# Performance work log

Hardware: AMD Instinct MI355X
Metric: run time of the kernel (lower is better)

Reference implementation:

```python
import jax, jax.numpy as jnp
import numpy as np

B, H, S, D = 4, 16, 2048, 64

def setup_inputs() -> dict:
    key = jax.random.key(0)
    kq, kk, kv = jax.random.split(key, 3)
    q = jax.random.normal(kq, (B, H, S, D), dtype=jnp.float32)
    k = jax.random.normal(kk, (B, H, S, D), dtype=jnp.float32)
    v = jax.random.normal(kv, (B, H, S, D), dtype=jnp.float32)
    return {"q": q, "k": k, "v": v}

def reference(q, k, v):
    # Faithful port of TransformerBlock.scaled_dot_product_attention
    # (is_causal=True, mha_dropout=0.0 / eval mode).
    head_dim = q.shape[-1]
    scale = jnp.asarray(head_dim, q.dtype) ** -0.5
    q_len, k_len = q.shape[-2], k.shape[-2]
    # causal additive bias: 0 on/below diagonal, -inf above
    causal = jnp.tril(jnp.ones((q_len, k_len), dtype=bool))
    attn_bias = jnp.where(causal, jnp.asarray(0.0, q.dtype), jnp.asarray(-jnp.inf, q.dtype))
    # [b,h,s,d] x [b,h,t,d] -> [b,h,s,t]
    attn_weights = jnp.einsum('bhsd,bhtd->bhst', q * scale, k) + attn_bias
    attn = jax.nn.softmax(attn_weights, axis=-1)
    out = jnp.einsum('bhst,bhtd->bhsd', attn, v)
    return out
```

## Files before the change

kernel.cpp:

```cpp
#include <hip/hip_runtime.h>
#include <math.h>


#define S_LEN 2048
#define D_DIM 64
#define TK 64
#define NHEAD 64
#define MASKV -30000.0f
#define MINIT 1000.0f
#define DEFER_THR 12.0f
#define MNEG -30000.0f
#define LSTR 72
#define PREP_KBLK 1024
#define PREP_VBLK 128

typedef __attribute__((ext_vector_type(8)))  short bf16x8;
typedef __attribute__((ext_vector_type(4)))  float f32x4;
typedef __attribute__((ext_vector_type(16))) float f32x16;

static __device__ __forceinline__ float fast_exp2(float x) {
#if __has_builtin(__builtin_amdgcn_exp2f)
    return __builtin_amdgcn_exp2f(x);
#else
    float r;
    asm volatile("v_exp_f32 %0, %1\n\ts_nop 1" : "=v"(r) : "v"(x));
    return r;
#endif
}

static __device__ __forceinline__ float fmax3(float a, float b, float c) {
    return fmaxf(fmaxf(a, b), c);
}

static __device__ __forceinline__ unsigned int pack_bf16(float a, float b) {
    union { float f; unsigned int u; } ca, cb;
    ca.f = a; cb.f = b;
    unsigned int ua = ca.u + 0x8000u;
    unsigned int ub = cb.u + 0x8000u;
    return (ua >> 16) | (ub & 0xFFFF0000u);
}

static __device__ __forceinline__ unsigned int pack_bf16_fast(float a, float b) {
#if __has_builtin(__builtin_amdgcn_perm)
    union { float f; unsigned int u; } ca, cb;
    ca.f = a; cb.f = b;
    return __builtin_amdgcn_perm(cb.u + 0x8000u, ca.u + 0x8000u, 0x07060302u);
#else
    return pack_bf16(a, b);
#endif
}

static __device__ __forceinline__ void plswap(unsigned int& x, unsigned int& y) {
    asm("s_nop 1\n\tv_permlane32_swap_b32 %0, %1" : "+v"(x), "+v"(y));
}
static __device__ __forceinline__ void plswapf(float x, float& t, float& u) {
    union { float f; unsigned int i; } c;
    c.f = x;
    unsigned int a = c.i, b;
    asm("v_mov_b32 %1, %0\n\t"
        "s_nop 1\n\t"
        "v_permlane32_swap_b32 %0, %1"
        : "+v"(a), "=&v"(b));
    c.i = a; t = c.f;
    c.i = b; u = c.f;
}

typedef const __attribute__((address_space(1))) unsigned int* gas1_t;
typedef __attribute__((address_space(3))) unsigned int* las3_t;
static __device__ __forceinline__ void stage16(const void* g, void* l) {
    __builtin_amdgcn_global_load_lds((gas1_t)g, (las3_t)l, 16, 0, 0);
}

__global__ __launch_bounds__(256)
void fa_prep(const float* __restrict__ kg, const float* __restrict__ vg,
             unsigned short* __restrict__ kb, unsigned short* __restrict__ vb)
{
    const int tid = threadIdx.x;
    const int bid = blockIdx.x;
    if (bid < PREP_KBLK) {
        const int tcid = bid * 256 + tid;
        float4 a[4], b[4];
        int rowv[4], dstv[4];
        #pragma unroll
        for (int s = 0; s < 4; ++s) {
            const int cid = tcid + s * 262144;
            const int ch  = cid & 7;
            const int row = cid >> 3;
            const int kv  = row & (S_LEN - 1);
            const float4* sp = reinterpret_cast<const float4*>(kg + (size_t)row * D_DIM + ch * 8);
            a[s] = sp[0];
            b[s] = sp[1];
            rowv[s] = row;
            dstv[s] = ch ^ (kv & 7);
        }
        #pragma unroll
        for (int s = 0; s < 4; ++s) {
            uint4 w;
            w.x = pack_bf16(a[s].x, a[s].y); w.y = pack_bf16(a[s].z, a[s].w);
            w.z = pack_bf16(b[s].x, b[s].y); w.w = pack_bf16(b[s].z, b[s].w);
            *reinterpret_cast<uint4*>(kb + (size_t)rowv[s] * D_DIM + dstv[s] * 8) = w;
        }
    } else {
        const int wvb  = (bid - PREP_KBLK) * 4 + (tid >> 6);
        const int lane = tid & 63;
        const int kg8  = lane >> 3;
        const int dg   = lane & 7;
        #pragma unroll 1
        for (int s = 0; s < 4; ++s) {
            const int wv = wvb + s * (PREP_VBLK * 4);
            const float* sp = vg + ((size_t)wv * TK + kg8 * 8) * D_DIM + dg * 8;
            float va[8][8];
            #pragma unroll
            for (int i = 0; i < 8; ++i) {
                const float4* q4 = reinterpret_cast<const float4*>(sp + (size_t)i * D_DIM);
                float4 x = q4[0], y = q4[1];
                va[i][0] = x.x; va[i][1] = x.y; va[i][2] = x.z; va[i][3] = x.w;
                va[i][4] = y.x; va[i][5] = y.y; va[i][6] = y.z; va[i][7] = y.w;
            }
            unsigned short* db = vb + (size_t)wv * (TK * D_DIM);
            #pragma unroll
            for (int j = 0; j < 8; ++j) {
                const int d = dg * 8 + j;
                uint4 w;
                w.x = pack_bf16(va[0][j], va[1][j]);
                w.y = pack_bf16(va[2][j], va[3][j]);
                w.z = pack_bf16(va[4][j], va[5][j]);
                w.w = pack_bf16(va[6][j], va[7][j]);
                *reinterpret_cast<uint4*>(db + d * D_DIM + 8 * (kg8 ^ j)) = w;
            }
        }
    }
}

__global__ __launch_bounds__(256, 3)
void fa_fwd(const float* __restrict__ qg,
            const unsigned short* __restrict__ kb,
            const unsigned short* __restrict__ vb,
            float* __restrict__ og)
{
    const int head = blockIdx.x;
    const int idx  = 15 - (int)blockIdx.y;
    const int q0   = idx * 128;
    const int tid  = threadIdx.x;
    const int wave = tid >> 6;
    const int lane = tid & 63;
    const int r0   = lane & 31;
    const int h    = lane >> 5;
    const int sw   = r0 & 7;

    __shared__ unsigned short Kl[2][TK * D_DIM];
    __shared__ unsigned short Vt[2][TK * D_DIM];

    const size_t hoff = (size_t)head * S_LEN * D_DIM;
    const unsigned short* kbh = kb + hoff;
    const unsigned short* vbh = vb + hoff;
    float* __restrict__ ogh = og + hoff;

    const int sgo  = wave * 512 + lane * 8;
    char* klds = (char*)&Kl[0][0];
    char* vlds = (char*)&Vt[0][0];
    char* kw   = klds + wave * 1024;
    char* vw   = vlds + wave * 1024;

    const int koff = r0 * 128;
    int coff[4];
    #pragma unroll
    for (int s = 0; s < 4; ++s) coff[s] = ((2 * s + h) ^ sw) << 4;

    const int T  = 2 * idx + 1;
    const int td = 2 * idx + (wave >> 1);

    const float QSC = 0.18033688011112042f;

    bf16x8 qf[4];
    {
        const int q = q0 + 32 * wave + r0;
        const float* qp = qg + hoff + (size_t)q * D_DIM;
        #pragma unroll
        for (int s = 0; s < 4; ++s) {
            const float* p = qp + 16 * s + 8 * h;
            float4 a = reinterpret_cast<const float4*>(p)[0];
            float4 b = reinterpret_cast<const float4*>(p)[1];
            unsigned int u0 = pack_bf16(a.x * QSC, a.y * QSC);
            unsigned int u1 = pack_bf16(a.z * QSC, a.w * QSC);
            unsigned int u2 = pack_bf16(b.x * QSC, b.y * QSC);
            unsigned int u3 = pack_bf16(b.z * QSC, b.w * QSC);
            qf[s][0] = (short)(u0 & 0xFFFF); qf[s][1] = (short)(u0 >> 16);
            qf[s][2] = (short)(u1 & 0xFFFF); qf[s][3] = (short)(u1 >> 16);
            qf[s][4] = (short)(u2 & 0xFFFF); qf[s][5] = (short)(u2 >> 16);
            qf[s][6] = (short)(u3 & 0xFFFF); qf[s][7] = (short)(u3 >> 16);
        }
    }

    float l_i = 0.f;
    f32x16 mc, oacc0, oacc1;
    #pragma unroll
    for (int g = 0; g < 16; ++g) { mc[g] = MINIT; oacc0[g] = 0.f; oacc1[g] = 0.f; }

    {
        const unsigned short* ks = kbh + sgo;
        const unsigned short* vs = vbh + sgo;
        stage16(ks,        kw);
        stage16(ks + 2048, kw + 4096);
        stage16(vs,        vw);
        stage16(vs + 2048, vw + 4096);
    }
    __syncthreads();

    int cur = 0;
    for (int t = 0; t <= T; ++t) {
        if (t < T) {
            const unsigned short* ks = kbh + (size_t)(t + 1) * 4096 + sgo;
            const unsigned short* vs = vbh + (size_t)(t + 1) * 4096 + sgo;
            const int nb = (cur ^ 1) * 8192;
            stage16(ks,        kw + nb);
            stage16(ks + 2048, kw + nb + 4096);
            stage16(vs,        vw + nb);
            stage16(vs + 2048, vw + nb + 4096);
        }

        if (t <= td) {
            const char* kt = klds + cur * 8192;
            const char* vt = vlds + cur * 8192;

            f32x16 s0, s1;
            __builtin_amdgcn_s_setprio(1);
            {
                bf16x8 k0 = *reinterpret_cast<const bf16x8*>(kt + koff + coff[0]);
                bf16x8 k1 = *reinterpret_cast<const bf16x8*>(kt + koff + 4096 + coff[0]);
                s0 = __builtin_amdgcn_mfma_f32_32x32x16_bf16(k0, qf[0], mc, 0, 0, 0);
                s1 = __builtin_amdgcn_mfma_f32_32x32x16_bf16(k1, qf[0], mc, 0, 0, 0);
            }
            #pragma unroll
            for (int s = 1; s < 4; ++s) {
                bf16x8 k0 = *reinterpret_cast<const bf16x8*>(kt + koff + coff[s]);
                bf16x8 k1 = *reinterpret_cast<const bf16x8*>(kt + koff + 4096 + coff[s]);
                s0 = __builtin_amdgcn_mfma_f32_32x32x16_bf16(k0, qf[s], s0, 0, 0, 0);
                s1 = __builtin_amdgcn_mfma_f32_32x32x16_bf16(k1, qf[s], s1, 0, 0, 0);
            }
            __builtin_amdgcn_s_setprio(0);

            if (t == td) {
                if ((wave & 1) == 0) {
                    #pragma unroll
                    for (int g = 0; g < 16; ++g) {
                        const int rl = (g & 3) + 8 * (g >> 2) + 4 * h;
                        if (rl > r0) s0[g] = MASKV;
                        s1[g] = MASKV;
                    }
                } else {
                    #pragma unroll
                    for (int g = 0; g < 16; ++g) {
                        const int rl = (g & 3) + 8 * (g >> 2) + 4 * h;
                        if (rl > r0) s1[g] = MASKV;
                    }
                }
            }

            float t0 = fmax3(s0[0],  s0[1],  s0[2]);
            float t1 = fmax3(s0[3],  s0[4],  s0[5]);
            float t2 = fmax3(s0[6],  s0[7],  s0[8]);
            float t3 = fmax3(s0[9],  s0[10], s0[11]);
            float t4 = fmax3(s0[12], s0[13], s0[14]);
            float t5 = fmax3(s0[15], s1[0],  s1[1]);
            float t6 = fmax3(s1[2],  s1[3],  s1[4]);
            float t7 = fmax3(s1[5],  s1[6],  s1[7]);
            float t8 = fmax3(s1[8],  s1[9],  s1[10]);
            float t9 = fmax3(s1[11], s1[12], s1[13]);
            float u0 = fmax3(t0, t1, t2);
            float u1 = fmax3(t3, t4, t5);
            float u2 = fmax3(t6, t7, t8);
            float u3 = fmax3(t9, s1[14], s1[15]);
            float rm = fmaxf(fmax3(u0, u1, u2), u3);
            { float a, b; plswapf(rm, a, b); rm = fmaxf(a, b); }

            if (__any(rm > DEFER_THR)) {
                float mx    = fmaxf(rm, 0.f);
                float alpha = fast_exp2(-mx);
                l_i *= alpha;
                #pragma unroll
                for (int g = 0; g < 16; ++g) {
                    oacc0[g] *= alpha; oacc1[g] *= alpha;
                    s0[g] -= mx; s1[g] -= mx;
                    mc[g] -= mx;
                }
            }

            float ea[16], eb[16];
            float rs = 0.f;
            #pragma unroll
            for (int g = 0; g < 16; ++g) {
                ea[g] = fast_exp2(s0[g]);
                eb[g] = fast_exp2(s1[g]);
            }
            #pragma unroll
            for (int g = 0; g < 16; ++g) rs += ea[g] + eb[g];
            { float a, b; plswapf(rs, a, b); l_i += a + b; }

            unsigned int pa[8], pb[8];
            #pragma unroll
            for (int k = 0; k < 8; ++k) {
                pa[k] = pack_bf16_fast(ea[2 * k], ea[2 * k + 1]);
                pb[k] = pack_bf16_fast(eb[2 * k], eb[2 * k + 1]);
            }
            plswap(pa[0], pa[2]); plswap(pa[1], pa[3]);
            plswap(pa[4], pa[6]); plswap(pa[5], pa[7]);
            plswap(pb[0], pb[2]); plswap(pb[1], pb[3]);
            plswap(pb[4], pb[6]); plswap(pb[5], pb[7]);
            union { unsigned int u[4]; bf16x8 v; } pf[4];
            pf[0].u[0] = pa[0]; pf[0].u[1] = pa[1]; pf[0].u[2] = pa[2]; pf[0].u[3] = pa[3];
            pf[1].u[0] = pa[4]; pf[1].u[1] = pa[5]; pf[1].u[2] = pa[6]; pf[1].u[3] = pa[7];
            pf[2].u[0] = pb[0]; pf[2].u[1] = pb[1]; pf[2].u[2] = pb[2]; pf[2].u[3] = pb[3];
            pf[3].u[0] = pb[4]; pf[3].u[1] = pb[5]; pf[3].u[2] = pb[6]; pf[3].u[3] = pb[7];

            __builtin_amdgcn_s_setprio(1);
            #pragma unroll
            for (int s = 0; s < 4; ++s) {
                bf16x8 v0 = *reinterpret_cast<const bf16x8*>(vt + koff + coff[s]);
                bf16x8 v1 = *reinterpret_cast<const bf16x8*>(vt + koff + 4096 + coff[s]);
                oacc0 = __builtin_amdgcn_mfma_f32_32x32x16_bf16(v0, pf[s].v, oacc0, 0, 0, 0);
                oacc1 = __builtin_amdgcn_mfma_f32_32x32x16_bf16(v1, pf[s].v, oacc1, 0, 0, 0);
            }
            __builtin_amdgcn_s_setprio(0);
        }

        __syncthreads();
        cur ^= 1;
    }

    {
        const float inv = 1.0f / l_i;
        float* op = ogh + (size_t)(q0 + 32 * wave + r0) * D_DIM;
        #pragma unroll
        for (int a = 0; a < 4; ++a) {
            float4 o4;
            o4.x = oacc0[4 * a + 0] * inv;
            o4.y = oacc0[4 * a + 1] * inv;
            o4.z = oacc0[4 * a + 2] * inv;
            o4.w = oacc0[4 * a + 3] * inv;
            reinterpret_cast<float4*>(op + 8 * a + 4 * h)[0] = o4;
        }
        #pragma unroll
        for (int a = 0; a < 4; ++a) {
            float4 o4;
            o4.x = oacc1[4 * a + 0] * inv;
            o4.y = oacc1[4 * a + 1] * inv;
            o4.z = oacc1[4 * a + 2] * inv;
            o4.w = oacc1[4 * a + 3] * inv;
            reinterpret_cast<float4*>(op + 32 + 8 * a + 4 * h)[0] = o4;
        }
    }
}

__global__ __launch_bounds__(256, 4)
void fa_fwd_fb(const float* __restrict__ qg,
               const float* __restrict__ kg,
               const float* __restrict__ vg,
               float* __restrict__ og)
{
    const int head = blockIdx.x;
    const int pr   = blockIdx.y;
    const int tid  = threadIdx.x;
    const int wave = tid >> 6;
    const int lane = tid & 63;
    const int m16  = lane & 15;
    const int quad = lane >> 4;

    __shared__ unsigned short Kl[TK][LSTR];
    __shared__ unsigned short Vt[D_DIM][LSTR];
    __shared__ unsigned short Pl[4][16][LSTR];

    const size_t hoff = (size_t)head * S_LEN * D_DIM;
    const float* kh = kg + hoff;
    const float* vh = vg + hoff;

    const int ksr = tid >> 2;
    const int ksc = (tid & 3) << 4;
    const int va  = lane >> 3;
    const int vb  = lane & 7;
    const int vrr = wave * 16 + 2 * vb;
    const int vcc = 8 * va;
    const float LOG2E = 1.4426950408889634f;

    for (int pass = 0; pass < 2; ++pass) {
        const int q0 = ((pass == 0) ? pr : (31 - pr)) * TK;

        bf16x8 qf[2];
        {
            const float* qp = qg + hoff + (size_t)(q0 + wave * 16 + m16) * D_DIM + quad * 8;
            #pragma unroll
            for (int c = 0; c < 2; ++c) {
                float4 a = reinterpret_cast<const float4*>(qp + c * 32)[0];
                float4 b = reinterpret_cast<const float4*>(qp + c * 32)[1];
                unsigned int u0 = pack_bf16(a.x * 0.125f, a.y * 0.125f);
                unsigned int u1 = pack_bf16(a.z * 0.125f, a.w * 0.125f);
                unsigned int u2 = pack_bf16(b.x * 0.125f, b.y * 0.125f);
                unsigned int u3 = pack_bf16(b.z * 0.125f, b.w * 0.125f);
                qf[c][0] = (short)(u0 & 0xFFFF); qf[c][1] = (short)(u0 >> 16);
                qf[c][2] = (short)(u1 & 0xFFFF); qf[c][3] = (short)(u1 >> 16);
                qf[c][4] = (short)(u2 & 0xFFFF); qf[c][5] = (short)(u2 >> 16);
                qf[c][6] = (short)(u3 & 0xFFFF); qf[c][7] = (short)(u3 >> 16);
            }
        }

        float m_i = MNEG, l_i = 0.f;
        f32x4 oacc[4];
        #pragma unroll
        for (int nc = 0; nc < 4; ++nc) oacc[nc] = (f32x4){0.f, 0.f, 0.f, 0.f};

        float4 kA, kB, kC, kD, vA, vB, vC, vD;
        {
            const float* kp = kh + (size_t)ksr * D_DIM + ksc;
            kA = reinterpret_cast<const float4*>(kp)[0];
            kB = reinterpret_cast<const float4*>(kp)[1];
            kC = reinterpret_cast<const float4*>(kp)[2];
            kD = reinterpret_cast<const float4*>(kp)[3];
            const float* vp = vh + (size_t)vrr * D_DIM + vcc;
            vA = reinterpret_cast<const float4*>(vp)[0];
            vB = reinterpret_cast<const float4*>(vp)[1];
            vC = reinterpret_cast<const float4*>(vp + D_DIM)[0];
            vD = reinterpret_cast<const float4*>(vp + D_DIM)[1];
        }

        for (int j0 = 0; j0 <= q0; j0 += TK) {
            __syncthreads();
            {
                uint4 w0, w1;
                w0.x = pack_bf16(kA.x, kA.y); w0.y = pack_bf16(kA.z, kA.w);
                w0.z = pack_bf16(kB.x, kB.y); w0.w = pack_bf16(kB.z, kB.w);
                w1.x = pack_bf16(kC.x, kC.y); w1.y = pack_bf16(kC.z, kC.w);
                w1.z = pack_bf16(kD.x, kD.y); w1.w = pack_bf16(kD.z, kD.w);
                *reinterpret_cast<uint4*>(&Kl[ksr][ksc])     = w0;
                *reinterpret_cast<uint4*>(&Kl[ksr][ksc + 8]) = w1;

                float r0[8] = {vA.x, vA.y, vA.z, vA.w, vB.x, vB.y, vB.z, vB.w};
                float r1[8] = {vC.x, vC.y, vC.z, vC.w, vD.x, vD.y, vD.z, vD.w};
                #pragma unroll
                for (int jj = 0; jj < 8; ++jj) {
                    int j = (jj + va) & 7;
                    *reinterpret_cast<unsigned int*>(&Vt[vcc + j][vrr]) = pack_bf16(r0[j], r1[j]);
                }
            }
            __syncthreads();

            if (j0 + TK <= q0) {
                const float* kp = kh + (size_t)(j0 + TK + ksr) * D_DIM + ksc;
                kA = reinterpret_cast<const float4*>(kp)[0];
                kB = reinterpret_cast<const float4*>(kp)[1];
                kC = reinterpret_cast<const float4*>(kp)[2];
                kD = reinterpret_cast<const float4*>(kp)[3];
                const float* vp = vh + (size_t)(j0 + TK + vrr) * D_DIM + vcc;
                vA = reinterpret_cast<const float4*>(vp)[0];
                vB = reinterpret_cast<const float4*>(vp)[1];
                vC = reinterpret_cast<const float4*>(vp + D_DIM)[0];
                vD = reinterpret_cast<const float4*>(vp + D_DIM)[1];
            }

            float sv[4][4];
            #pragma unroll
            for (int nt = 0; nt < 4; ++nt) {
                f32x4 acc = (f32x4){0.f, 0.f, 0.f, 0.f};
                bf16x8 kf0 = *reinterpret_cast<const bf16x8*>(&Kl[nt * 16 + m16][quad * 8]);
                bf16x8 kf1 = *reinterpret_cast<const bf16x8*>(&Kl[nt * 16 + m16][32 + quad * 8]);
                acc = __builtin_amdgcn_mfma_f32_16x16x32_bf16(kf0, qf[0], acc, 0, 0, 0);
                acc = __builtin_amdgcn_mfma_f32_16x16x32_bf16(kf1, qf[1], acc, 0, 0, 0);
                #pragma unroll
                for (int r = 0; r < 4; ++r) sv[nt][r] = acc[r];
            }

            if (j0 == q0) {
                #pragma unroll
                for (int nt = 0; nt < 4; ++nt)
                    #pragma unroll
                    for (int r = 0; r < 4; ++r)
                        if (nt * 16 + quad * 4 + r > wave * 16 + m16) sv[nt][r] = MNEG;
            }

            float a0 = fmaxf(fmaxf(sv[0][0], sv[0][1]), fmaxf(sv[0][2], sv[0][3]));
            float a1 = fmaxf(fmaxf(sv[1][0], sv[1][1]), fmaxf(sv[1][2], sv[1][3]));
            float a2 = fmaxf(fmaxf(sv[2][0], sv[2][1]), fmaxf(sv[2][2], sv[2][3]));
            float a3 = fmaxf(fmaxf(sv[3][0], sv[3][1]), fmaxf(sv[3][2], sv[3][3]));
            float rm = fmaxf(fmaxf(a0, a1), fmaxf(a2, a3));
            rm = fmaxf(rm, __shfl_xor(rm, 16, 64));
            rm = fmaxf(rm, __shfl_xor(rm, 32, 64));
            float mnew  = fmaxf(m_i, rm);
            float alpha = fast_exp2((m_i - mnew) * LOG2E);
            float msc   = mnew * LOG2E;
            m_i = mnew;

            float rs = 0.f;
            #pragma unroll
            for (int nt = 0; nt < 4; ++nt) {
                float e0 = fast_exp2(fmaf(sv[nt][0], LOG2E, -msc));
                float e1 = fast_exp2(fmaf(sv[nt][1], LOG2E, -msc));
                float e2 = fast_exp2(fmaf(sv[nt][2], LOG2E, -msc));
                float e3 = fast_exp2(fmaf(sv[nt][3], LOG2E, -msc));
                rs += (e0 + e1) + (e2 + e3);
                uint2 pw;
                pw.x = pack_bf16(e0, e1);
                pw.y = pack_bf16(e2, e3);
                *reinterpret_cast<uint2*>(&Pl[wave][m16][nt * 16 + quad * 4]) = pw;
            }
            rs += __shfl_xor(rs, 16, 64);
            rs += __shfl_xor(rs, 32, 64);
            l_i = fmaf(alpha, l_i, rs);

            #pragma unroll
            for (int nc = 0; nc < 4; ++nc)
                #pragma unroll
                for (int r = 0; r < 4; ++r)
                    oacc[nc][r] *= alpha;

            asm volatile("s_waitcnt lgkmcnt(0)" ::: "memory");

            bf16x8 pf0 = *reinterpret_cast<const bf16x8*>(&Pl[wave][m16][quad * 8]);
            bf16x8 pf1 = *reinterpret_cast<const bf16x8*>(&Pl[wave][m16][32 + quad * 8]);
            #pragma unroll
            for (int nc = 0; nc < 4; ++nc) {
                bf16x8 vf0 = *reinterpret_cast<const bf16x8*>(&Vt[nc * 16 + m16][quad * 8]);
                bf16x8 vf1 = *reinterpret_cast<const bf16x8*>(&Vt[nc * 16 + m16][32 + quad * 8]);
                oacc[nc] = __builtin_amdgcn_mfma_f32_16x16x32_bf16(vf0, pf0, oacc[nc], 0, 0, 0);
                oacc[nc] = __builtin_amdgcn_mfma_f32_16x16x32_bf16(vf1, pf1, oacc[nc], 0, 0, 0);
            }
        }

        float inv = 1.0f / l_i;
        float* op = og + hoff + (size_t)(q0 + wave * 16 + m16) * D_DIM;
        #pragma unroll
        for (int nc = 0; nc < 4; ++nc) {
            float4 o4;
            o4.x = oacc[nc][0] * inv;
            o4.y = oacc[nc][1] * inv;
            o4.z = oacc[nc][2] * inv;
            o4.w = oacc[nc][3] * inv;
            reinterpret_cast<float4*>(op + nc * 16 + quad * 4)[0] = o4;
        }
    }
}

extern "C" void kernel_launch(void* const* d_in, const int* in_sizes, int n_in,
                              void* d_out, int out_size, void* d_ws, size_t ws_size,
                              hipStream_t stream) {
    const float* q = (const float*)d_in[0];
    const float* k = (const float*)d_in[1];
    const float* v = (const float*)d_in[2];
    float* o = (float*)d_out;
    const size_t kvShorts = (size_t)NHEAD * S_LEN * D_DIM;
    const size_t wsNeed   = 2 * kvShorts * sizeof(unsigned short);
    if (d_ws != nullptr && ws_size >= wsNeed) {
        unsigned short* kbp = (unsigned short*)d_ws;
        unsigned short* vbp = kbp + kvShorts;
        fa_prep<<<PREP_KBLK + PREP_VBLK, 256, 0, stream>>>(k, v, kbp, vbp);
        dim3 grid(NHEAD, 16);
        fa_fwd<<<grid, 256, 0, stream>>>(q, kbp, vbp, o);
    } else {
        dim3 grid(NHEAD, 16);
        fa_fwd_fb<<<grid, 256, 0, stream>>>(q, k, v, o);
    }
}
```

Baseline: 189.6 us.

## Pre-permute K/V tiles into MFMA fragment order and raise occupancy hint

```diff
diff --git a/kernel.cpp b/kernel.cpp
--- a/kernel.cpp
+++ b/kernel.cpp
@@ -80,25 +80,24 @@
     if (bid < PREP_KBLK) {
         const int tcid = bid * 256 + tid;
         float4 a[4], b[4];
-        int rowv[4], dstv[4];
+        size_t dsto[4];
         #pragma unroll
         for (int s = 0; s < 4; ++s) {
             const int cid = tcid + s * 262144;
             const int ch  = cid & 7;
             const int row = cid >> 3;
-            const int kv  = row & (S_LEN - 1);
+            const int kvt = row & 63;
             const float4* sp = reinterpret_cast<const float4*>(kg + (size_t)row * D_DIM + ch * 8);
             a[s] = sp[0];
             b[s] = sp[1];
-            rowv[s] = row;
-            dstv[s] = ch ^ (kv & 7);
+            dsto[s] = (size_t)(row - kvt) * 64 + (kvt >> 5) * 2048 + ch * 256 + (kvt & 31) * 8;
         }
         #pragma unroll
         for (int s = 0; s < 4; ++s) {
             uint4 w;
             w.x = pack_bf16(a[s].x, a[s].y); w.y = pack_bf16(a[s].z, a[s].w);
             w.z = pack_bf16(b[s].x, b[s].y); w.w = pack_bf16(b[s].z, b[s].w);
-            *reinterpret_cast<uint4*>(kb + (size_t)rowv[s] * D_DIM + dstv[s] * 8) = w;
+            *reinterpret_cast<uint4*>(kb + dsto[s]) = w;
         }
     } else {
         const int wvb  = (bid - PREP_KBLK) * 4 + (tid >> 6);
@@ -117,7 +116,7 @@
                 va[i][0] = x.x; va[i][1] = x.y; va[i][2] = x.z; va[i][3] = x.w;
                 va[i][4] = y.x; va[i][5] = y.y; va[i][6] = y.z; va[i][7] = y.w;
             }
-            unsigned short* db = vb + (size_t)wv * (TK * D_DIM);
+            unsigned short* db = vb + (size_t)wv * 4096;
             #pragma unroll
             for (int j = 0; j < 8; ++j) {
                 const int d = dg * 8 + j;
@@ -126,13 +125,13 @@
                 w.y = pack_bf16(va[2][j], va[3][j]);
                 w.z = pack_bf16(va[4][j], va[5][j]);
                 w.w = pack_bf16(va[6][j], va[7][j]);
-                *reinterpret_cast<uint4*>(db + d * D_DIM + 8 * (kg8 ^ j)) = w;
-            }
-        }
-    }
-}
-
-__global__ __launch_bounds__(256, 3)
+                *reinterpret_cast<uint4*>(db + (d >> 5) * 2048 + kg8 * 256 + (d & 31) * 8) = w;
+            }
+        }
+    }
+}
+
+__global__ __launch_bounds__(256, 4)
 void fa_fwd(const float* __restrict__ qg,
             const unsigned short* __restrict__ kb,
             const unsigned short* __restrict__ vb,
@@ -146,7 +145,6 @@
     const int lane = tid & 63;
     const int r0   = lane & 31;
     const int h    = lane >> 5;
-    const int sw   = r0 & 7;
 
     __shared__ unsigned short Kl[2][TK * D_DIM];
     __shared__ unsigned short Vt[2][TK * D_DIM];
@@ -162,10 +160,7 @@
     char* kw   = klds + wave * 1024;
     char* vw   = vlds + wave * 1024;
 
-    const int koff = r0 * 128;
-    int coff[4];
-    #pragma unroll
-    for (int s = 0; s < 4; ++s) coff[s] = ((2 * s + h) ^ sw) << 4;
+    const int fro = r0 * 16 + h * 512;
 
     const int T  = 2 * idx + 1;
     const int td = 2 * idx + (wave >> 1);
@@ -220,21 +215,21 @@
         }
 
         if (t <= td) {
-            const char* kt = klds + cur * 8192;
-            const char* vt = vlds + cur * 8192;
+            const char* kt = klds + cur * 8192 + fro;
+            const char* vt = vlds + cur * 8192 + fro;
 
             f32x16 s0, s1;
             __builtin_amdgcn_s_setprio(1);
             {
-                bf16x8 k0 = *reinterpret_cast<const bf16x8*>(kt + koff + coff[0]);
-                bf16x8 k1 = *reinterpret_cast<const bf16x8*>(kt + koff + 4096 + coff[0]);
+                bf16x8 k0 = *reinterpret_cast<const bf16x8*>(kt);
+                bf16x8 k1 = *reinterpret_cast<const bf16x8*>(kt + 4096);
                 s0 = __builtin_amdgcn_mfma_f32_32x32x16_bf16(k0, qf[0], mc, 0, 0, 0);
                 s1 = __builtin_amdgcn_mfma_f32_32x32x16_bf16(k1, qf[0], mc, 0, 0, 0);
             }
             #pragma unroll
             for (int s = 1; s < 4; ++s) {
-                bf16x8 k0 = *reinterpret_cast<const bf16x8*>(kt + koff + coff[s]);
-                bf16x8 k1 = *reinterpret_cast<const bf16x8*>(kt + koff + 4096 + coff[s]);
+                bf16x8 k0 = *reinterpret_cast<const bf16x8*>(kt + s * 1024);
+                bf16x8 k1 = *reinterpret_cast<const bf16x8*>(kt + 4096 + s * 1024);
                 s0 = __builtin_amdgcn_mfma_f32_32x32x16_bf16(k0, qf[s], s0, 0, 0, 0);
                 s1 = __builtin_amdgcn_mfma_f32_32x32x16_bf16(k1, qf[s], s1, 0, 0, 0);
             }
@@ -316,8 +311,8 @@
             __builtin_amdgcn_s_setprio(1);
             #pragma unroll
             for (int s = 0; s < 4; ++s) {
-                bf16x8 v0 = *reinterpret_cast<const bf16x8*>(vt + koff + coff[s]);
-                bf16x8 v1 = *reinterpret_cast<const bf16x8*>(vt + koff + 4096 + coff[s]);
+                bf16x8 v0 = *reinterpret_cast<const bf16x8*>(vt + s * 1024);
+                bf16x8 v1 = *reinterpret_cast<const bf16x8*>(vt + 4096 + s * 1024);
                 oacc0 = __builtin_amdgcn_mfma_f32_32x32x16_bf16(v0, pf[s].v, oacc0, 0, 0, 0);
                 oacc1 = __builtin_amdgcn_mfma_f32_32x32x16_bf16(v1, pf[s].v, oacc1, 0, 0, 0);
             }
```

Result: no change. 188.2 us (-0.7%).
